# Kernel optimization log

Measured on AMD Instinct MI355X. Metric: run time of the kernel, lower is better.

The kernel has to match this reference:

```python
import jax, jax.numpy as jnp
from jax import lax
import numpy as np

DN = ('NCHW', 'OIHW', 'NCHW')
K = 5          # downsample_kernel_size
S = 2          # scale_factor
M = 64         # m_channels


def setup_inputs() -> dict:
    key = jax.random.key(0)
    k0, k1, k2 = jax.random.split(key, 3)
    B, C, H, W = 8, 256, 128, 128
    x = jax.random.normal(k0, (B, C, H, W), jnp.float32)
    # compress_conv: 1x1, C -> M
    w1 = jax.random.normal(k1, (M, C, 1, 1), jnp.float32) * (1.0 / np.sqrt(C))
    b1 = jnp.zeros((M,), jnp.float32)
    # encoder_conv: 3x3, M -> K*K, stride S, pad 1
    w2 = jax.random.normal(k2, (K * K, M, 3, 3), jnp.float32) * (1.0 / np.sqrt(M * 9))
    b2 = jnp.zeros((K * K,), jnp.float32)
    return {"x": x, "w1": w1, "b1": b1, "w2": w2, "b2": b2}


def reference(x, w1, b1, w2, b2):
    B, C, H, W = x.shape
    nH, nW = H // S, W // S
    # kernel prediction branch
    ker = lax.conv_general_dilated(x, w1, (1, 1), 'VALID', dimension_numbers=DN)
    ker = ker + b1[None, :, None, None]
    ker = lax.conv_general_dilated(ker, w2, (S, S), ((1, 1), (1, 1)), dimension_numbers=DN)
    ker = ker + b2[None, :, None, None]          # (B, K*K, nH, nW)
    ker = jax.nn.softmax(ker, axis=1)
    # unfold: (B, C*K*K, nH, nW), channel-major patch ordering (matches torch Unfold)
    pad = K // 2
    patches = lax.conv_general_dilated_patches(
        x, (K, K), (S, S), ((pad, pad), (pad, pad)), dimension_numbers=DN)
    patches = patches.reshape(B, C, K * K, nH, nW)
    # softmax-weighted sum over the K*K window per output pixel
    return jnp.einsum('bckhw,bkhw->bchw', patches, ker)
```

## Files before the change

kernel.cpp:

```cpp
#include <hip/hip_runtime.h>
#include <hip/hip_bf16.h>

#define Bq 8
#define Cq 256
#define Hq 128
#define Wq 128
#define Mq 64
#define KK 25
#define NH 64
#define NW 64
#define HWq (Hq*Wq)
#define NHW (NH*NW)

typedef __attribute__((ext_vector_type(8))) short short8;
typedef __attribute__((ext_vector_type(4))) float f32x4;

__device__ __forceinline__ unsigned short f2b(float f) {
  __hip_bfloat16 h = __float2bfloat16(f);
  return __builtin_bit_cast(unsigned short, h);
}

#define XPAD 72
__global__ __launch_bounds__(256) void conv1x1_mfma(
    const float* __restrict__ x, const float* __restrict__ w1,
    const float* __restrict__ b1, float* __restrict__ t1) {
  __shared__ unsigned short xs[128 * XPAD];
  __shared__ unsigned short ws[64 * XPAD];
  const int tid  = threadIdx.x;
  const int lane = tid & 63;
  const int wv   = tid >> 6;
  const int P0   = blockIdx.x << 7;
  const int b    = P0 >> 14;
  const int hw0  = P0 & (HWq - 1);

  const int quad = lane >> 4;
  const int l15  = lane & 15;

  const int sc  = tid >> 2;
  const int sp0 = (tid & 3) * 4;
  const int wm  = tid >> 2;
  const int wc0 = (tid & 3) * 16;

  f32x4 acc[4][2];
#pragma unroll
  for (int mt = 0; mt < 4; ++mt)
#pragma unroll
    for (int nt = 0; nt < 2; ++nt) acc[mt][nt] = (f32x4)0.f;

  for (int cc = 0; cc < 4; ++cc) {
    __syncthreads();
    const float* xgc = x + ((size_t)b * Cq + cc * 64 + sc) * HWq + hw0 + sp0;
#pragma unroll
    for (int i = 0; i < 8; ++i) {
      float4 v = *(const float4*)(xgc + i * 16);
      int px = sp0 + i * 16;
      xs[(px + 0) * XPAD + sc] = f2b(v.x);
      xs[(px + 1) * XPAD + sc] = f2b(v.y);
      xs[(px + 2) * XPAD + sc] = f2b(v.z);
      xs[(px + 3) * XPAD + sc] = f2b(v.w);
    }
    const float* wgc = w1 + wm * Cq + cc * 64 + wc0;
#pragma unroll
    for (int u = 0; u < 4; ++u) {
      float4 v = *(const float4*)(wgc + u * 4);
      unsigned short* d = &ws[wm * XPAD + wc0 + u * 4];
      d[0] = f2b(v.x); d[1] = f2b(v.y); d[2] = f2b(v.z); d[3] = f2b(v.w);
    }
    __syncthreads();
#pragma unroll
    for (int ks = 0; ks < 2; ++ks) {
      const int c0 = ks * 32 + quad * 8;
      short8 af[4], bfr[2];
#pragma unroll
      for (int mt = 0; mt < 4; ++mt)
        af[mt] = *(const short8*)&ws[(mt * 16 + l15) * XPAD + c0];
#pragma unroll
      for (int nt = 0; nt < 2; ++nt)
        bfr[nt] = *(const short8*)&xs[(wv * 32 + nt * 16 + l15) * XPAD + c0];
#pragma unroll
      for (int mt = 0; mt < 4; ++mt)
#pragma unroll
        for (int nt = 0; nt < 2; ++nt)
          acc[mt][nt] = __builtin_amdgcn_mfma_f32_16x16x32_bf16(
              af[mt], bfr[nt], acc[mt][nt], 0, 0, 0);
    }
  }
#pragma unroll
  for (int mt = 0; mt < 4; ++mt) {
#pragma unroll
    for (int r = 0; r < 4; ++r) {
      int m = mt * 16 + quad * 4 + r;
      float bv = b1[m];
#pragma unroll
      for (int nt = 0; nt < 2; ++nt) {
        int px = wv * 32 + nt * 16 + l15;
        t1[((size_t)b * Mq + m) * HWq + hw0 + px] = acc[mt][nt][r] + bv;
      }
    }
  }
}

__global__ __launch_bounds__(512) void encoder_kernel(
    const float* __restrict__ t1, const float* __restrict__ w2,
    const float* __restrict__ b2, float* __restrict__ ker) {
  __shared__ float red[8][KK][64];
  const int tid = threadIdx.x;
  const int ow  = tid & 63;
  const int mg  = tid >> 6;
  const int b   = blockIdx.x >> 6;
  const int oh  = blockIdx.x & 63;

  float acc[KK];
#pragma unroll
  for (int k = 0; k < KK; ++k) acc[k] = 0.f;

  const float* tb = t1 + (size_t)b * Mq * HWq;
  const int iwb = 2 * ow - 1;

  for (int mi = 0; mi < 8; ++mi) {
    const int m = __builtin_amdgcn_readfirstlane(mg * 8 + mi);
    const float* tm = tb + (size_t)m * HWq;
    const float* wm = w2 + m * 9;
#pragma unroll
    for (int dh = 0; dh < 3; ++dh) {
      int ih = 2 * oh + dh - 1;
      if ((unsigned)ih < (unsigned)Hq) {
        const float* tr = tm + ih * Wq;
        float v0 = (ow > 0) ? tr[iwb] : 0.f;
        float v1 = tr[iwb + 1];
        float v2 = tr[iwb + 2];
        const float* wr = wm + dh * 3;
#pragma unroll
        for (int k = 0; k < KK; ++k) {
          acc[k] += v0 * wr[k * 576 + 0];
          acc[k] += v1 * wr[k * 576 + 1];
          acc[k] += v2 * wr[k * 576 + 2];
        }
      }
    }
  }
#pragma unroll
  for (int k = 0; k < KK; ++k) red[mg][k][ow] = acc[k];
  __syncthreads();
  if (tid < 64) {
    float lg[KK];
#pragma unroll
    for (int k = 0; k < KK; ++k) {
      float s = b2[k];
#pragma unroll
      for (int g = 0; g < 8; ++g) s += red[g][k][tid];
      lg[k] = s;
    }
    float mx = lg[0];
#pragma unroll
    for (int k = 1; k < KK; ++k) mx = fmaxf(mx, lg[k]);
    float s = 0.f;
#pragma unroll
    for (int k = 0; k < KK; ++k) { lg[k] = __expf(lg[k] - mx); s += lg[k]; }
    float inv = 1.f / s;
    float* kb = ker + (size_t)b * KK * NHW + oh * NW + tid;
#pragma unroll
    for (int k = 0; k < KK; ++k) kb[k * NHW] = lg[k] * inv;
  }
}

__global__ __launch_bounds__(256) void reassemble_kernel(
    const float* __restrict__ x, const float* __restrict__ ker,
    float* __restrict__ out) {
  __shared__ float klds[2][KK][64];
  const int tid = threadIdx.x;
  const int bid = blockIdx.x;
  const int c8  = bid & 7;
  const int ohp = (bid >> 3) & 31;
  const int b   = bid >> 8;
  const int oh0 = 2 * ohp;

  for (int i = tid; i < 2 * KK * 64; i += 256) {
    int rr  = i / 1600;
    int rem = i - rr * 1600;
    int k   = rem >> 6;
    int owi = rem & 63;
    klds[rr][k][owi] = ker[(size_t)(b * KK + k) * NHW + (oh0 + rr) * NW + owi];
  }
  __syncthreads();

  const int ow = tid & 63;
  const int cs = tid >> 6;
  float kr0[KK], kr1[KK];
#pragma unroll
  for (int k = 0; k < KK; ++k) { kr0[k] = klds[0][k][ow]; kr1[k] = klds[1][k][ow]; }

  const int r0  = 4 * ohp - 2;
  const int iwb = 2 * ow - 2;
  const bool e0 = (iwb >= 0);
  const bool e4 = (iwb + 4 < Wq);
  const float2 z2 = make_float2(0.f, 0.f);

  for (int ci = 0; ci < 8; ++ci) {
    int c = c8 * 32 + cs * 8 + ci;
    const float* xc = x + (size_t)(b * Cq + c) * HWq;
    float a0 = 0.f, a1 = 0.f;
#pragma unroll
    for (int j = 0; j < 7; ++j) {
      int ih = r0 + j;
      bool rok = (unsigned)ih < (unsigned)Hq;
      const float* xr = xc + ih * Wq;
      float2 v01 = (rok && e0) ? *(const float2*)(xr + iwb)     : z2;
      float2 v23 = rok         ? *(const float2*)(xr + iwb + 2) : z2;
      float  v4  = (rok && e4) ? xr[iwb + 4] : 0.f;
      if (j < 5) {
        a0 += v01.x * kr0[j*5+0]; a0 += v01.y * kr0[j*5+1];
        a0 += v23.x * kr0[j*5+2]; a0 += v23.y * kr0[j*5+3];
        a0 += v4    * kr0[j*5+4];
      }
      if (j >= 2) {
        int dy = j - 2;
        a1 += v01.x * kr1[dy*5+0]; a1 += v01.y * kr1[dy*5+1];
        a1 += v23.x * kr1[dy*5+2]; a1 += v23.y * kr1[dy*5+3];
        a1 += v4    * kr1[dy*5+4];
      }
    }
    float* op = out + (size_t)(b * Cq + c) * NHW + oh0 * NW + ow;
    op[0]  = a0;
    op[NW] = a1;
  }
}

extern "C" void kernel_launch(void* const* d_in, const int* in_sizes, int n_in,
                              void* d_out, int out_size, void* d_ws, size_t ws_size,
                              hipStream_t stream) {
  const float* x  = (const float*)d_in[0];
  const float* w1 = (const float*)d_in[1];
  const float* b1 = (const float*)d_in[2];
  const float* w2 = (const float*)d_in[3];
  const float* b2 = (const float*)d_in[4];
  float* out = (float*)d_out;

  float* t1  = (float*)d_ws;
  float* ker = t1 + (size_t)Bq * Mq * HWq;

  conv1x1_mfma<<<1024, 256, 0, stream>>>(x, w1, b1, t1);
  encoder_kernel<<<Bq * NH, 512, 0, stream>>>(t1, w2, b2, ker);
  reassemble_kernel<<<2048, 256, 0, stream>>>(x, ker, out);
}
```

Before: 315.0 us.

## Stage x row slabs in LDS for reassembly to cut overlapping window reloads

Reassemble blocks are retiled to cover 8 output rows by 8 channels. Each block first copies a padded 19-row input slab per channel into shared memory with vectorized loads, and the softmax kernel weights are read straight into registers. This lowers redundant global reads of x from overlapping 5x5 stride-2 windows and removes row-bound checks from the inner loop. In exchange it needs about 78KB of LDS per block, which limits occupancy, and the load phase cannot overlap with compute.

```diff
diff --git a/kernel.cpp b/kernel.cpp
--- a/kernel.cpp
+++ b/kernel.cpp
@@ -164,50 +164,67 @@
   }
 }
 
+#define RSL_ROWS 19
+#define RSL_CSZ  (RSL_ROWS * Wq)
 __global__ __launch_bounds__(256) void reassemble_kernel(
     const float* __restrict__ x, const float* __restrict__ ker,
     float* __restrict__ out) {
-  __shared__ float klds[2][KK][64];
+  __shared__ float xsl[8 * RSL_CSZ + 8];
   const int tid = threadIdx.x;
   const int bid = blockIdx.x;
-  const int c8  = bid & 7;
-  const int ohp = (bid >> 3) & 31;
+  const int cg  = bid & 31;
+  const int ohg = (bid >> 5) & 7;
   const int b   = bid >> 8;
-  const int oh0 = 2 * ohp;
-
-  for (int i = tid; i < 2 * KK * 64; i += 256) {
-    int rr  = i / 1600;
-    int rem = i - rr * 1600;
-    int k   = rem >> 6;
-    int owi = rem & 63;
-    klds[rr][k][owi] = ker[(size_t)(b * KK + k) * NHW + (oh0 + rr) * NW + owi];
-  }
+  const int r0  = 16 * ohg - 2;
+
+  const int zlo = (r0 < 0) ? -r0 : 0;
+  const int zhi = (r0 + RSL_ROWS > Hq) ? (r0 + RSL_ROWS - Hq) : 0;
+  if (zlo > 0) {
+    for (int c = 0; c < 8; ++c)
+      for (int i = tid; i < zlo * Wq; i += 256) xsl[c * RSL_CSZ + i] = 0.f;
+  }
+  if (zhi > 0) {
+    for (int c = 0; c < 8; ++c)
+      for (int i = tid; i < zhi * Wq; i += 256)
+        xsl[c * RSL_CSZ + (RSL_ROWS - zhi) * Wq + i] = 0.f;
+  }
+  const int vs = (r0 > 0) ? r0 : 0;
+  const int ve = (r0 + RSL_ROWS < Hq) ? (r0 + RSL_ROWS) : Hq;
+  const int nvec = ((ve - vs) * Wq) >> 2;
+  const int loff = (vs - r0) * Wq;
+  for (int c = 0; c < 8; ++c) {
+    const float* g = x + ((size_t)(b * Cq + cg * 8 + c)) * HWq + vs * Wq;
+    float* d = xsl + c * RSL_CSZ + loff;
+    for (int i = tid; i < nvec; i += 256) {
+      float4 v = *(const float4*)(g + 4 * i);
+      *(float4*)(d + 4 * i) = v;
+    }
+  }
+
+  const int ow = tid & 63;
+  const int rq = tid >> 6;
+  const int oh = 8 * ohg + 2 * rq;
+  float kr0[KK], kr1[KK];
+  const float* kb = ker + (size_t)b * KK * NHW + oh * NW + ow;
+#pragma unroll
+  for (int k = 0; k < KK; ++k) { kr0[k] = kb[k * NHW]; kr1[k] = kb[k * NHW + NW]; }
+
   __syncthreads();
 
-  const int ow = tid & 63;
-  const int cs = tid >> 6;
-  float kr0[KK], kr1[KK];
-#pragma unroll
-  for (int k = 0; k < KK; ++k) { kr0[k] = klds[0][k][ow]; kr1[k] = klds[1][k][ow]; }
-
-  const int r0  = 4 * ohp - 2;
-  const int iwb = 2 * ow - 2;
-  const bool e0 = (iwb >= 0);
-  const bool e4 = (iwb + 4 < Wq);
+  const int jb = 4 * rq;
+  const bool e0 = (ow > 0);
+  const bool e4 = (ow < 63);
   const float2 z2 = make_float2(0.f, 0.f);
 
-  for (int ci = 0; ci < 8; ++ci) {
-    int c = c8 * 32 + cs * 8 + ci;
-    const float* xc = x + (size_t)(b * Cq + c) * HWq;
+  for (int c = 0; c < 8; ++c) {
+    const float* sl = xsl + c * RSL_CSZ;
     float a0 = 0.f, a1 = 0.f;
 #pragma unroll
     for (int j = 0; j < 7; ++j) {
-      int ih = r0 + j;
-      bool rok = (unsigned)ih < (unsigned)Hq;
-      const float* xr = xc + ih * Wq;
-      float2 v01 = (rok && e0) ? *(const float2*)(xr + iwb)     : z2;
-      float2 v23 = rok         ? *(const float2*)(xr + iwb + 2) : z2;
-      float  v4  = (rok && e4) ? xr[iwb + 4] : 0.f;
+      const float* xr = sl + (jb + j) * Wq + 2 * ow - 2;
+      float2 v01 = e0 ? *(const float2*)xr : z2;
+      float2 v23 = *(const float2*)(xr + 2);
+      float  v4  = e4 ? xr[4] : 0.f;
       if (j < 5) {
         a0 += v01.x * kr0[j*5+0]; a0 += v01.y * kr0[j*5+1];
         a0 += v23.x * kr0[j*5+2]; a0 += v23.y * kr0[j*5+3];
@@ -220,7 +237,7 @@
         a1 += v4    * kr1[dy*5+4];
       }
     }
-    float* op = out + (size_t)(b * Cq + c) * NHW + oh0 * NW + ow;
+    float* op = out + ((size_t)(b * Cq + cg * 8 + c)) * NHW + oh * NW + ow;
     op[0]  = a0;
     op[NW] = a1;
   }
```

After: 301.4 us. 4.3% less time.
